# Kernel tuning notes

Measured on AMD Instinct MI355X. Metric: run time of the kernel, lower is better.

The kernel has to match this reference:

```python
import jax, jax.numpy as jnp
import numpy as np

S, B, D, H, FF, L, V, O = 512, 32, 512, 8, 2048, 6, 32000, 1000
DH = D // H
EPS = 1e-5


def layer_norm(x, g, b):
    mu = jnp.mean(x, axis=-1, keepdims=True)
    var = jnp.mean((x - mu) ** 2, axis=-1, keepdims=True)
    return (x - mu) * jax.lax.rsqrt(var + EPS) * g + b


def positional_encoding(seq_len, dim):
    pos = np.arange(seq_len, dtype=np.float32)[:, None]
    i = np.arange(dim)
    angle = pos / (10000.0 ** ((i // 2 * 2.0) / dim))
    pe = np.where(i % 2 == 0, np.sin(angle), np.cos(angle)).astype(np.float32)
    return jnp.asarray(pe)  # [seq_len, dim]


def setup_inputs() -> dict:
    key = jax.random.key(0)
    ks = jax.random.split(key, 16)
    sc = 0.02
    inp = {
        'x': jax.random.randint(ks[0], (S, B), 0, V, dtype=jnp.int32),
        'x_len': jnp.full((B,), S, dtype=jnp.int32),
        'emb': jax.random.normal(ks[1], (V, D), jnp.float32) * sc,
        'Wq': jax.random.normal(ks[2], (L, D, D), jnp.float32) * sc,
        'bq': jnp.zeros((L, D), jnp.float32),
        'Wk': jax.random.normal(ks[3], (L, D, D), jnp.float32) * sc,
        'bk': jnp.zeros((L, D), jnp.float32),
        'Wv': jax.random.normal(ks[4], (L, D, D), jnp.float32) * sc,
        'bv': jnp.zeros((L, D), jnp.float32),
        'Wo': jax.random.normal(ks[5], (L, D, D), jnp.float32) * sc,
        'bo': jnp.zeros((L, D), jnp.float32),
        'ln1_g': jnp.ones((L, D), jnp.float32),
        'ln1_b': jnp.zeros((L, D), jnp.float32),
        'W1': jax.random.normal(ks[6], (L, D, FF), jnp.float32) * sc,
        'b1': jnp.zeros((L, FF), jnp.float32),
        'W2': jax.random.normal(ks[7], (L, FF, D), jnp.float32) * sc,
        'b2': jnp.zeros((L, D), jnp.float32),
        'ln2_g': jnp.ones((L, D), jnp.float32),
        'ln2_b': jnp.zeros((L, D), jnp.float32),
        'W_fc': jax.random.normal(ks[8], (S * D, O), jnp.float32) * sc,
        'b_fc': jnp.zeros((O,), jnp.float32),
    }
    return inp


def reference(x, x_len, emb, Wq, bq, Wk, bk, Wv, bv, Wo, bo, ln1_g, ln1_b,
              W1, b1, W2, b2, ln2_g, ln2_b, W_fc, b_fc):
    out = emb[x]                      # [S, B, D]
    out = jnp.transpose(out, (1, 0, 2))  # [B, S, D]
    out = out + positional_encoding(S, D)[None, :, :]
    scale = DH ** -0.5
    for l in range(L):
        # NOTE: faithful to the original buggy head-split: plain row-major
        # reshape [B,S,D] -> [B*H,S,DH] without a [B,H,S,DH] transpose.
        q = jnp.reshape(out @ Wq[l] + bq[l], (B * H, S, DH))
        k = jnp.reshape(out @ Wk[l] + bk[l], (B * H, S, DH))
        v = jnp.reshape(out @ Wv[l] + bv[l], (B * H, S, DH))
        attn = jax.nn.softmax(jnp.einsum('gqd,gkd->gqk', q, k) * scale, axis=-1)
        ctx = jnp.einsum('gqk,gkd->gqd', attn, v).reshape(B, S, D)
        h = layer_norm(ctx @ Wo[l] + bo[l] + out, ln1_g[l], ln1_b[l])
        f = jax.nn.relu(h @ W1[l] + b1[l]) @ W2[l] + b2[l]
        out = layer_norm(f + h, ln2_g[l], ln2_b[l])
    out = out.reshape(B, S * D)
    return out @ W_fc + b_fc          # [B, O]
```

## Files before the change

### kernel.cpp

```cpp
#include <hip/hip_runtime.h>
#include <cstdint>
#include <cstddef>

#define S_  512
#define B_  32
#define D_  512
#define FF_ 2048
#define L_  6
#define O_  1000
#define M_  (B_*S_)
#define G_  256
#define DH_ 64

typedef __attribute__((ext_vector_type(8))) short bf16x8;
typedef __attribute__((ext_vector_type(4))) float f32x4;
typedef __attribute__((ext_vector_type(16))) float f32x16;

__device__ __forceinline__ unsigned short f2bf(float f) {
  unsigned int u = __builtin_bit_cast(unsigned int, f);
  u = (u + 0x7fffu + ((u >> 16) & 1u)) >> 16;
  return (unsigned short)u;
}
__device__ __forceinline__ float bf2f(unsigned short u) {
  return __builtin_bit_cast(float, (unsigned int)u << 16);
}
__device__ __forceinline__ unsigned int pkbf(float a, float b) {
  return (unsigned int)f2bf(a) | ((unsigned int)f2bf(b) << 16);
}
__device__ __forceinline__ unsigned int prm(float a, float b) {
  return __builtin_amdgcn_perm(__builtin_bit_cast(unsigned int, b),
                               __builtin_bit_cast(unsigned int, a), 0x07060302u);
}
__device__ __forceinline__ void gload_lds16(const void* g, void* l) {
  __builtin_amdgcn_global_load_lds(
      (const __attribute__((address_space(1))) unsigned int*)g,
      (__attribute__((address_space(3))) unsigned int*)l, 16, 0, 0);
}

__global__ void pe_kernel(float* __restrict__ pe) {
  int i = blockIdx.x * 256 + threadIdx.x;
  int s = i >> 9, d = i & 511;
  double de = (double)(d & ~1);
  double ang = (double)s * exp(de * (-9.210340371976184 / 512.0));
  pe[i] = (d & 1) ? (float)cos(ang) : (float)sin(ang);
}

__global__ void wconv_kernel(const float* __restrict__ W, unsigned short* __restrict__ Wt,
                             int K, int N, size_t ozs) {
  __shared__ float tile[32][33];
  const float* Wl = W + (size_t)blockIdx.z * K * N;
  unsigned short* Wtl = Wt + (size_t)blockIdx.z * ozs;
  int k0 = blockIdx.x * 32, n0 = blockIdx.y * 32;
  int c = threadIdx.x & 31, rb = threadIdx.x >> 5;
#pragma unroll
  for (int i = 0; i < 4; ++i) {
    int r = rb + i * 8;
    tile[r][c] = Wl[(size_t)(k0 + r) * N + n0 + c];
  }
  __syncthreads();
#pragma unroll
  for (int i = 0; i < 4; ++i) {
    int r = rb + i * 8;
    Wtl[(size_t)(n0 + r) * K + k0 + c] = f2bf(tile[c][r]);
  }
}

__global__ void embed_kernel(const int* __restrict__ x, const float* __restrict__ emb,
                             const float* __restrict__ pe, unsigned short* __restrict__ xb) {
  int bi = blockIdx.x;
  int s = bi / B_, b = bi % B_;
  int tok = x[s * B_ + b];
  int d = threadIdx.x * 4;
  float4 e = *(const float4*)(emb + (size_t)tok * D_ + d);
  float4 p = *(const float4*)(pe + (size_t)s * D_ + d);
  size_t o = ((size_t)b * S_ + s) * D_ + d;
  ushort4 u;
  u.x = f2bf(e.x + p.x); u.y = f2bf(e.y + p.y);
  u.z = f2bf(e.z + p.z); u.w = f2bf(e.w + p.w);
  *(ushort4*)(xb + o) = u;
}

__global__ __launch_bounds__(256, 2) void gemm_kernel(
    const unsigned short* __restrict__ A, const unsigned short* __restrict__ Bt,
    const float* __restrict__ b0, const float* __restrict__ b1, const float* __restrict__ b2,
    unsigned short* __restrict__ o0, unsigned short* __restrict__ o1, unsigned short* __restrict__ o2,
    int K, int N, int relu, int split, int nbx) {
  __shared__ unsigned short As[3][128 * 32];
  __shared__ unsigned short Bs[3][256 * 32];
  int nwg = nbx * (M_ / 128);
  int cpx = nwg >> 3;
  int id = blockIdx.x;
  int wg = (id & 7) * cpx + (id >> 3);
  int bx = wg % nbx, by = wg / nbx;
  int m0 = by * 128, n0 = bx * 256;

  int tid = threadIdx.x, lane = tid & 63, wid = tid >> 6;
  f32x4 acc[8][4];
#pragma unroll
  for (int mi = 0; mi < 8; ++mi)
#pragma unroll
    for (int ni = 0; ni < 4; ++ni) acc[mi][ni] = (f32x4)0.0f;

  int srow = lane >> 2, scol = (lane & 3) * 8;
  const unsigned short* Abase = A + (size_t)m0 * K;
  const unsigned short* Bbase = Bt + (size_t)n0 * K;
  int c16 = lane & 15, hi = lane >> 4;
  int koff = hi * 8;
  int brow = wid * 64 + c16;
  int nk = K >> 5;

  auto STAGE = [&](int kt, int bb) {
    int k0 = kt * 32;
#pragma unroll
    for (int i = 0; i < 6; ++i) {
      int c = wid * 6 + i;
      if (c < 8) {
        gload_lds16(Abase + (size_t)(c * 16 + srow) * K + k0 + scol, (char*)As[bb] + c * 1024);
      } else {
        int c2 = c - 8;
        gload_lds16(Bbase + (size_t)(c2 * 16 + srow) * K + k0 + scol, (char*)Bs[bb] + c2 * 1024);
      }
    }
  };

  STAGE(0, 0); STAGE(1, 1); STAGE(2, 2);
  int bb = 0;
  for (int kt = 0; kt < nk; ++kt) {
    int rem = nk - 1 - kt;
    if (rem >= 2)      asm volatile("s_waitcnt vmcnt(12)" ::: "memory");
    else if (rem == 1) asm volatile("s_waitcnt vmcnt(6)" ::: "memory");
    else               asm volatile("s_waitcnt vmcnt(0)" ::: "memory");
    __builtin_amdgcn_s_barrier();
    __builtin_amdgcn_sched_barrier(0);
    bf16x8 af[8], bfr[4];
#pragma unroll
    for (int mi = 0; mi < 8; ++mi) af[mi] = *(const bf16x8*)&As[bb][(mi * 16 + c16) * 32 + koff];
#pragma unroll
    for (int ni = 0; ni < 4; ++ni) bfr[ni] = *(const bf16x8*)&Bs[bb][(brow + ni * 16) * 32 + koff];
    __builtin_amdgcn_s_setprio(1);
#pragma unroll
    for (int mi = 0; mi < 8; ++mi)
#pragma unroll
      for (int ni = 0; ni < 4; ++ni)
        acc[mi][ni] = __builtin_amdgcn_mfma_f32_16x16x32_bf16(bfr[ni], af[mi], acc[mi][ni], 0, 0, 0);
    __builtin_amdgcn_s_setprio(0);
    __builtin_amdgcn_sched_barrier(0);
    __builtin_amdgcn_s_barrier();
    if (kt + 3 < nk) STAGE(kt + 3, bb);
    bb = (bb == 2) ? 0 : bb + 1;
  }

  const float* bias = b0;
  unsigned short* outb = o0;
  int nbase = n0, ostride = N;
  if (split) {
    int seg = n0 >> 9;
    if (seg == 1) { bias = b1; outb = o1; }
    else if (seg == 2) { bias = b2; outb = o2; }
    nbase = n0 & 511; ostride = 512;
  }
#pragma unroll
  for (int ni = 0; ni < 4; ++ni) {
    int colb = nbase + wid * 64 + ni * 16 + hi * 4;
    float4 bv = *(const float4*)(bias + colb);
#pragma unroll
    for (int mi = 0; mi < 8; ++mi) {
      int row = m0 + mi * 16 + c16;
      float v0 = acc[mi][ni][0] + bv.x;
      float v1 = acc[mi][ni][1] + bv.y;
      float v2 = acc[mi][ni][2] + bv.z;
      float v3 = acc[mi][ni][3] + bv.w;
      if (relu) { v0 = fmaxf(v0, 0.f); v1 = fmaxf(v1, 0.f); v2 = fmaxf(v2, 0.f); v3 = fmaxf(v3, 0.f); }
      *(uint2*)(outb + (size_t)row * ostride + colb) = make_uint2(pkbf(v0, v1), pkbf(v2, v3));
    }
  }
}

__global__ __launch_bounds__(256, 2) void gemm128_kernel(
    const unsigned short* __restrict__ A, const unsigned short* __restrict__ Bt,
    const float* __restrict__ bias, unsigned short* __restrict__ outb,
    int K, int N, int nbx) {
  __shared__ unsigned short As[3][128 * 32];
  __shared__ unsigned short Bs[3][128 * 32];
  int nwg = nbx * (M_ / 128);
  int cpx = nwg >> 3;
  int id = blockIdx.x;
  int wg = (id & 7) * cpx + (id >> 3);
  int bx = wg % nbx, by = wg / nbx;
  int m0 = by * 128, n0 = bx * 128;

  int tid = threadIdx.x, lane = tid & 63, wid = tid >> 6;
  int wm = wid >> 1, wn = wid & 1;
  f32x4 acc[4][4];
#pragma unroll
  for (int mi = 0; mi < 4; ++mi)
#pragma unroll
    for (int ni = 0; ni < 4; ++ni) acc[mi][ni] = (f32x4)0.0f;

  int srow = lane >> 2, scol = (lane & 3) * 8;
  const unsigned short* Abase = A + (size_t)m0 * K;
  const unsigned short* Bbase = Bt + (size_t)n0 * K;
  int c16 = lane & 15, hi = lane >> 4;
  int koff = hi * 8;
  int arow = wm * 64 + c16, brow = wn * 64 + c16;
  int nk = K >> 5;

  auto STAGE = [&](int kt, int bb) {
    int k0 = kt * 32;
#pragma unroll
    for (int i = 0; i < 2; ++i) {
      int c = wid * 2 + i;
      gload_lds16(Abase + (size_t)(c * 16 + srow) * K + k0 + scol, (char*)As[bb] + c * 1024);
      gload_lds16(Bbase + (size_t)(c * 16 + srow) * K + k0 + scol, (char*)Bs[bb] + c * 1024);
    }
  };

  STAGE(0, 0); STAGE(1, 1); STAGE(2, 2);
  int bb = 0;
  for (int kt = 0; kt < nk; ++kt) {
    int rem = nk - 1 - kt;
    if (rem >= 2)      asm volatile("s_waitcnt vmcnt(8)" ::: "memory");
    else if (rem == 1) asm volatile("s_waitcnt vmcnt(4)" ::: "memory");
    else               asm volatile("s_waitcnt vmcnt(0)" ::: "memory");
    __builtin_amdgcn_s_barrier();
    __builtin_amdgcn_sched_barrier(0);
    bf16x8 af[4], bfr[4];
#pragma unroll
    for (int mi = 0; mi < 4; ++mi) af[mi] = *(const bf16x8*)&As[bb][(arow + mi * 16) * 32 + koff];
#pragma unroll
    for (int ni = 0; ni < 4; ++ni) bfr[ni] = *(const bf16x8*)&Bs[bb][(brow + ni * 16) * 32 + koff];
    __builtin_amdgcn_s_setprio(1);
#pragma unroll
    for (int mi = 0; mi < 4; ++mi)
#pragma unroll
      for (int ni = 0; ni < 4; ++ni)
        acc[mi][ni] = __builtin_amdgcn_mfma_f32_16x16x32_bf16(bfr[ni], af[mi], acc[mi][ni], 0, 0, 0);
    __builtin_amdgcn_s_setprio(0);
    __builtin_amdgcn_sched_barrier(0);
    __builtin_amdgcn_s_barrier();
    if (kt + 3 < nk) STAGE(kt + 3, bb);
    bb = (bb == 2) ? 0 : bb + 1;
  }

#pragma unroll
  for (int ni = 0; ni < 4; ++ni) {
    int colb = n0 + wn * 64 + ni * 16 + hi * 4;
    float4 bv = *(const float4*)(bias + colb);
#pragma unroll
    for (int mi = 0; mi < 4; ++mi) {
      int row = m0 + wm * 64 + mi * 16 + c16;
      float v0 = acc[mi][ni][0] + bv.x;
      float v1 = acc[mi][ni][1] + bv.y;
      float v2 = acc[mi][ni][2] + bv.z;
      float v3 = acc[mi][ni][3] + bv.w;
      *(uint2*)(outb + (size_t)row * N + colb) = make_uint2(pkbf(v0, v1), pkbf(v2, v3));
    }
  }
}

__global__ __launch_bounds__(128) void addln_kernel(
    const unsigned short* __restrict__ Y, const unsigned short* __restrict__ R,
    const float* __restrict__ g, const float* __restrict__ b,
    unsigned short* __restrict__ Out) {
  __shared__ float red[2], red2[2];
  int row = blockIdx.x, t = threadIdx.x;
  size_t o = (size_t)row * 512 + t * 4;
  ushort4 yv = *(const ushort4*)(Y + o);
  ushort4 rv = *(const ushort4*)(R + o);
  float v0 = bf2f(yv.x) + bf2f(rv.x);
  float v1 = bf2f(yv.y) + bf2f(rv.y);
  float v2 = bf2f(yv.z) + bf2f(rv.z);
  float v3 = bf2f(yv.w) + bf2f(rv.w);
  float s = v0 + v1 + v2 + v3;
#pragma unroll
  for (int m = 1; m < 64; m <<= 1) s += __shfl_xor(s, m);
  if ((t & 63) == 0) red[t >> 6] = s;
  __syncthreads();
  float mean = (red[0] + red[1]) * (1.0f / 512.0f);
  float d0 = v0 - mean, d1 = v1 - mean, d2 = v2 - mean, d3 = v3 - mean;
  float sq = d0 * d0 + d1 * d1 + d2 * d2 + d3 * d3;
#pragma unroll
  for (int m = 1; m < 64; m <<= 1) sq += __shfl_xor(sq, m);
  if ((t & 63) == 0) red2[t >> 6] = sq;
  __syncthreads();
  float var = (red2[0] + red2[1]) * (1.0f / 512.0f);
  float rstd = rsqrtf(var + 1e-5f);
  float4 gg = *(const float4*)(g + t * 4);
  float4 bb = *(const float4*)(b + t * 4);
  float y0 = d0 * rstd * gg.x + bb.x;
  float y1 = d1 * rstd * gg.y + bb.y;
  float y2 = d2 * rstd * gg.z + bb.z;
  float y3 = d3 * rstd * gg.w + bb.w;
  *(uint2*)(Out + o) = make_uint2(pkbf(y0, y1), pkbf(y2, y3));
}

__global__ __launch_bounds__(256) void attn_kernel(
    const unsigned short* __restrict__ Q, const unsigned short* __restrict__ Kb,
    const unsigned short* __restrict__ Vb, unsigned short* __restrict__ Ctx) {
  __shared__ char KlB[8192];
  __shared__ char VtB[8192];
  int g = blockIdx.y;
  int q0 = blockIdx.x * 256;
  const unsigned short* Kg = Kb + (size_t)g * 512 * 64;
  const unsigned short* Vg = Vb + (size_t)g * 512 * 64;
  int tid = threadIdx.x, lane = tid & 63, wid = tid >> 6;
  int l31 = lane & 31, h = lane >> 5;
  bool lo = (lane < 32);
  int qrowA = q0 + wid * 64 + l31;
  int qrowB = qrowA + 32;
  const float sc2 = 0.125f * 1.44269504f;

  bf16x8 qfa[4], qfb[4];
  {
    const unsigned short* qpa = Q + ((size_t)g * 512 + qrowA) * 64;
    const unsigned short* qpb = Q + ((size_t)g * 512 + qrowB) * 64;
#pragma unroll
    for (int c = 0; c < 4; ++c) {
      bf16x8 ra = *(const bf16x8*)(qpa + c * 16 + h * 8);
      bf16x8 rb = *(const bf16x8*)(qpb + c * 16 + h * 8);
      union { unsigned int u[4]; bf16x8 v; } ua, ub;
#pragma unroll
      for (int j = 0; j < 4; ++j) {
        ua.u[j] = pkbf(bf2f((unsigned short)ra[2 * j]) * sc2,
                       bf2f((unsigned short)ra[2 * j + 1]) * sc2);
        ub.u[j] = pkbf(bf2f((unsigned short)rb[2 * j]) * sc2,
                       bf2f((unsigned short)rb[2 * j + 1]) * sc2);
      }
      qfa[c] = ua.v; qfb[c] = ub.v;
    }
  }

  f32x16 cA0 = (f32x16)0.0f, cA1 = (f32x16)0.0f;
  f32x16 cB0 = (f32x16)0.0f, cB1 = (f32x16)0.0f;
  float mrA = -3.0e38f, lsA = 0.0f;
  float mrB = -3.0e38f, lsB = 0.0f;

  for (int kt = 0; kt < 8; ++kt) {
    __syncthreads();
    {
      int row = tid >> 2;
      size_t base = (size_t)(kt * 64 + row) * 64;
#pragma unroll
      for (int i = 0; i < 2; ++i) {
        int cb = ((tid & 3) + 4 * i) * 16;
        bf16x8 kv = *(const bf16x8*)(Kg + base + cb / 2);
        *(bf16x8*)(KlB + row * 128 + (cb ^ ((row & 7) << 4))) = kv;
        bf16x8 vv = *(const bf16x8*)(Vg + base + cb / 2);
#pragma unroll
        for (int j = 0; j < 8; ++j) {
          int d = cb / 2 + j;
          *(unsigned short*)(VtB + d * 128 + ((2 * row) ^ ((d & 7) << 4))) =
              (unsigned short)vv[j];
        }
      }
    }
    __syncthreads();

#pragma unroll
    for (int sub = 0; sub < 2; ++sub) {
      f32x16 s0 = (f32x16)0.0f, s1 = (f32x16)0.0f;
#pragma unroll
      for (int c = 0; c < 4; ++c) {
        int cb = 32 * c + 16 * h;
        int sw = cb ^ ((l31 & 7) << 4);
        bf16x8 k0 = *(const bf16x8*)(KlB + l31 * 128 + sw);
        bf16x8 k1 = *(const bf16x8*)(KlB + (32 + l31) * 128 + sw);
        bf16x8 qf = sub ? qfb[c] : qfa[c];
        s0 = __builtin_amdgcn_mfma_f32_32x32x16_bf16(k0, qf, s0, 0, 0, 0);
        s1 = __builtin_amdgcn_mfma_f32_32x32x16_bf16(k1, qf, s1, 0, 0, 0);
      }

      float mr = sub ? mrB : mrA;
      float ls = sub ? lsB : lsA;
      float pm = s0[0];
#pragma unroll
      for (int i = 1; i < 16; ++i) pm = fmaxf(pm, s0[i]);
#pragma unroll
      for (int i = 0; i < 16; ++i) pm = fmaxf(pm, s1[i]);
      pm = fmaxf(pm, __shfl_xor(pm, 32));
      if (!__all(pm <= mr + 8.0f)) {
        float mnew = fmaxf(mr, pm);
        float alpha = exp2f(mr - mnew);
        ls *= alpha;
        if (sub) {
#pragma unroll
          for (int i = 0; i < 16; ++i) { cB0[i] *= alpha; cB1[i] *= alpha; }
        } else {
#pragma unroll
          for (int i = 0; i < 16; ++i) { cA0[i] *= alpha; cA1[i] *= alpha; }
        }
        mr = mnew;
      }
      float p[32];
      float rs = 0.0f;
#pragma unroll
      for (int i = 0; i < 16; ++i) { p[i] = exp2f(s0[i] - mr); rs += p[i]; }
#pragma unroll
      for (int i = 0; i < 16; ++i) { p[16 + i] = exp2f(s1[i] - mr); rs += p[16 + i]; }
      float rso = __shfl_xor(rs, 32);
      ls += rs + rso;
      if (sub) { mrB = mr; lsB = ls; } else { mrA = mr; lsA = ls; }

      union { unsigned int u[4]; bf16x8 v; } pa[4];
#pragma unroll
      for (int t = 0; t < 2; ++t) {
#pragma unroll
        for (int u = 0; u < 2; ++u) {
#pragma unroll
          for (int pr = 0; pr < 2; ++pr) {
            const int b0i = t * 16 + 8 * u;
            unsigned int a  = prm(p[b0i + 2 * pr],     p[b0i + 2 * pr + 1]);
            unsigned int b  = prm(p[b0i + 4 + 2 * pr], p[b0i + 4 + 2 * pr + 1]);
            unsigned int sa = __shfl_xor(a, 32);
            unsigned int sb = __shfl_xor(b, 32);
            pa[t * 2 + u].u[pr]     = lo ? a  : sb;
            pa[t * 2 + u].u[2 + pr] = lo ? sa : b;
          }
        }
      }

#pragma unroll
      for (int kc = 0; kc < 4; ++kc) {
        int cb = 32 * kc + 16 * h;
        int sw = cb ^ ((l31 & 7) << 4);
        bf16x8 v0 = *(const bf16x8*)(VtB + l31 * 128 + sw);
        bf16x8 v1 = *(const bf16x8*)(VtB + (32 + l31) * 128 + sw);
        if (sub) {
          cB0 = __builtin_amdgcn_mfma_f32_32x32x16_bf16(v0, pa[kc].v, cB0, 0, 0, 0);
          cB1 = __builtin_amdgcn_mfma_f32_32x32x16_bf16(v1, pa[kc].v, cB1, 0, 0, 0);
        } else {
          cA0 = __builtin_amdgcn_mfma_f32_32x32x16_bf16(v0, pa[kc].v, cA0, 0, 0, 0);
          cA1 = __builtin_amdgcn_mfma_f32_32x32x16_bf16(v1, pa[kc].v, cA1, 0, 0, 0);
        }
      }
    }
  }

#pragma unroll
  for (int sub = 0; sub < 2; ++sub) {
    float inv = 1.0f / (sub ? lsB : lsA);
    int qrow = sub ? qrowB : qrowA;
    unsigned short* cp = Ctx + ((size_t)g * 512 + qrow) * 64;
#pragma unroll
    for (int dh = 0; dh < 2; ++dh) {
#pragma unroll
      for (int rq = 0; rq < 4; ++rq) {
        float e0 = (sub ? (dh ? cB1[rq * 4 + 0] : cB0[rq * 4 + 0]) : (dh ? cA1[rq * 4 + 0] : cA0[rq * 4 + 0])) * inv;
        float e1 = (sub ? (dh ? cB1[rq * 4 + 1] : cB0[rq * 4 + 1]) : (dh ? cA1[rq * 4 + 1] : cA0[rq * 4 + 1])) * inv;
        float e2 = (sub ? (dh ? cB1[rq * 4 + 2] : cB0[rq * 4 + 2]) : (dh ? cA1[rq * 4 + 2] : cA0[rq * 4 + 2])) * inv;
        float e3 = (sub ? (dh ? cB1[rq * 4 + 3] : cB0[rq * 4 + 3]) : (dh ? cA1[rq * 4 + 3] : cA0[rq * 4 + 3])) * inv;
        int d0 = dh * 32 + rq * 8 + h * 4;
        *(uint2*)(cp + d0) = make_uint2(pkbf(e0, e1), pkbf(e2, e3));
      }
    }
  }
}

#define KCH 1024
__global__ __launch_bounds__(512) void fc_part_kernel(const unsigned short* __restrict__ act,
                                                      const float* __restrict__ Wfc,
                                                      float* __restrict__ part) {
  __shared__ float al[32][256];
  int t = threadIdx.x;
  int kc = blockIdx.x;
  size_t k0 = (size_t)kc * KCH;
  int o1 = t;
  int o2 = 512 + t;
  bool a2 = (o2 < O_);
  float acc1[32], acc2[32];
#pragma unroll
  for (int bb = 0; bb < 32; ++bb) { acc1[bb] = 0.0f; acc2[bb] = 0.0f; }
  for (int sub = 0; sub < KCH / 256; ++sub) {
    __syncthreads();
    for (int i = t; i < 32 * 128; i += 512) {
      int bb = i >> 7, kk = (i & 127) * 2;
      ushort2 u = *(const ushort2*)(act + (size_t)bb * 262144 + k0 + sub * 256 + kk);
      al[bb][kk] = bf2f(u.x);
      al[bb][kk + 1] = bf2f(u.y);
    }
    __syncthreads();
    const float* wp = Wfc + (k0 + sub * 256) * O_;
    for (int kk = 0; kk < 256; kk += 4) {
      const float* wr = wp + (size_t)kk * O_;
      float w10 = wr[o1];
      float w11 = wr[O_ + o1];
      float w12 = wr[2 * O_ + o1];
      float w13 = wr[3 * O_ + o1];
      float w20 = a2 ? wr[o2] : 0.0f;
      float w21 = a2 ? wr[O_ + o2] : 0.0f;
      float w22 = a2 ? wr[2 * O_ + o2] : 0.0f;
      float w23 = a2 ? wr[3 * O_ + o2] : 0.0f;
#pragma unroll
      for (int bb = 0; bb < 32; ++bb) {
        f32x4 av = *(const f32x4*)&al[bb][kk];
        acc1[bb] = fmaf(av[0], w10, acc1[bb]);
        acc1[bb] = fmaf(av[1], w11, acc1[bb]);
        acc1[bb] = fmaf(av[2], w12, acc1[bb]);
        acc1[bb] = fmaf(av[3], w13, acc1[bb]);
        acc2[bb] = fmaf(av[0], w20, acc2[bb]);
        acc2[bb] = fmaf(av[1], w21, acc2[bb]);
        acc2[bb] = fmaf(av[2], w22, acc2[bb]);
        acc2[bb] = fmaf(av[3], w23, acc2[bb]);
      }
    }
  }
#pragma unroll
  for (int bb = 0; bb < 32; ++bb) {
    part[((size_t)kc * 32 + bb) * O_ + o1] = acc1[bb];
    if (a2) part[((size_t)kc * 32 + bb) * O_ + o2] = acc2[bb];
  }
}

__global__ void fc_reduce_kernel(const float* __restrict__ part, const float* __restrict__ bfc,
                                 float* __restrict__ out) {
  int o = blockIdx.x * 256 + threadIdx.x;
  int b = blockIdx.y;
  if (o >= O_) return;
  float s = bfc[o];
  for (int c = 0; c < 256; ++c) s += part[((size_t)c * 32 + b) * O_ + o];
  out[(size_t)b * O_ + o] = s;
}

extern "C" void kernel_launch(void* const* d_in, const int* in_sizes, int n_in,
                              void* d_out, int out_size, void* d_ws, size_t ws_size,
                              hipStream_t stream) {
  const int*   x   = (const int*)d_in[0];
  const float* emb = (const float*)d_in[2];
  const float* Wq  = (const float*)d_in[3];
  const float* bq  = (const float*)d_in[4];
  const float* Wk  = (const float*)d_in[5];
  const float* bk  = (const float*)d_in[6];
  const float* Wv  = (const float*)d_in[7];
  const float* bv  = (const float*)d_in[8];
  const float* Wo  = (const float*)d_in[9];
  const float* bo  = (const float*)d_in[10];
  const float* g1  = (const float*)d_in[11];
  const float* bn1 = (const float*)d_in[12];
  const float* W1  = (const float*)d_in[13];
  const float* bf1 = (const float*)d_in[14];
  const float* W2  = (const float*)d_in[15];
  const float* bf2 = (const float*)d_in[16];
  const float* g2  = (const float*)d_in[17];
  const float* bn2 = (const float*)d_in[18];
  const float* Wfc = (const float*)d_in[19];
  const float* bfc = (const float*)d_in[20];
  float* out = (float*)d_out;

  char* ws = (char*)d_ws;
  size_t off = 0;
  auto take = [&](size_t bytes) { char* p = ws + off; off += (bytes + 255) & ~(size_t)255; return p; };
  float*          pe   = (float*)take((size_t)512 * 512 * 4);
  unsigned short* wqkv = (unsigned short*)take((size_t)L_ * 1536 * 512 * 2);
  unsigned short* wot  = (unsigned short*)take((size_t)L_ * 512 * 512 * 2);
  unsigned short* w1t  = (unsigned short*)take((size_t)L_ * 2048 * 512 * 2);
  unsigned short* w2t  = (unsigned short*)take((size_t)L_ * 512 * 2048 * 2);
  unsigned short* xb   = (unsigned short*)take((size_t)M_ * 512 * 2);
  unsigned short* qb   = (unsigned short*)take((size_t)M_ * 512 * 2);
  unsigned short* kb   = (unsigned short*)take((size_t)M_ * 512 * 2);
  unsigned short* vb   = (unsigned short*)take((size_t)M_ * 512 * 2);
  unsigned short* cxb  = (unsigned short*)take((size_t)M_ * 512 * 2);
  unsigned short* hb   = (unsigned short*)take((size_t)M_ * 512 * 2);
  unsigned short* t1   = (unsigned short*)take((size_t)M_ * 512 * 2);
  unsigned short* f1b  = qb;
  float*          part = (float*)qb;

  pe_kernel<<<1024, 256, 0, stream>>>(pe);
  wconv_kernel<<<dim3(16, 16, L_), 256, 0, stream>>>(Wq, wqkv,          512, 512,  (size_t)1536 * 512);
  wconv_kernel<<<dim3(16, 16, L_), 256, 0, stream>>>(Wk, wqkv + 262144, 512, 512,  (size_t)1536 * 512);
  wconv_kernel<<<dim3(16, 16, L_), 256, 0, stream>>>(Wv, wqkv + 524288, 512, 512,  (size_t)1536 * 512);
  wconv_kernel<<<dim3(16, 16, L_), 256, 0, stream>>>(Wo, wot,           512, 512,  (size_t)512 * 512);
  wconv_kernel<<<dim3(16, 64, L_), 256, 0, stream>>>(W1, w1t,           512, 2048, (size_t)2048 * 512);
  wconv_kernel<<<dim3(64, 16, L_), 256, 0, stream>>>(W2, w2t,           2048, 512, (size_t)512 * 2048);
  embed_kernel<<<M_, 128, 0, stream>>>(x, emb, pe, xb);

  for (int l = 0; l < L_; ++l) {
    gemm_kernel<<<768, 256, 0, stream>>>(
        xb, wqkv + (size_t)l * 1536 * 512,
        bq + l * 512, bk + l * 512, bv + l * 512,
        qb, kb, vb, 512, 1536, 0, 1, 6);
    attn_kernel<<<dim3(2, G_), 256, 0, stream>>>(qb, kb, vb, cxb);
    gemm128_kernel<<<512, 256, 0, stream>>>(
        cxb, wot + (size_t)l * 512 * 512, bo + l * 512, t1, 512, 512, 4);
    addln_kernel<<<M_, 128, 0, stream>>>(t1, xb, g1 + l * 512, bn1 + l * 512, hb);
    gemm_kernel<<<1024, 256, 0, stream>>>(
        hb, w1t + (size_t)l * 2048 * 512,
        bf1 + l * 2048, nullptr, nullptr,
        f1b, nullptr, nullptr, 512, 2048, 1, 0, 8);
    gemm128_kernel<<<512, 256, 0, stream>>>(
        f1b, w2t + (size_t)l * 512 * 2048, bf2 + l * 512, t1, 2048, 512, 4);
    addln_kernel<<<M_, 128, 0, stream>>>(t1, hb, g2 + l * 512, bn2 + l * 512, xb);
  }

  fc_part_kernel<<<256, 512, 0, stream>>>(xb, Wfc, part);
  fc_reduce_kernel<<<dim3(4, 32), 256, 0, stream>>>(part, bfc, out);
}
```

Baseline: 1.915 ms.

## Use 128x128 double-buffered GEMM for QKV and prefetch K/V tiles in attention

Moves the split QKV projection from the 128x256 triple-buffered GEMM to the 128x128 kernel, which now uses double buffering and a three-blocks-per-CU launch bound, so more workgroups fit on the device. The attention kernel now loads the next K/V tile into registers while computing on the current one, which hides global-load latency behind the MFMA work. The trade-offs are a shallower prefetch pipeline in the GEMM, tighter register limits, and more registers held in attention.

```diff
diff --git a/kernel.cpp b/kernel.cpp
--- a/kernel.cpp
+++ b/kernel.cpp
@@ -82,9 +82,8 @@
 
 __global__ __launch_bounds__(256, 2) void gemm_kernel(
     const unsigned short* __restrict__ A, const unsigned short* __restrict__ Bt,
-    const float* __restrict__ b0, const float* __restrict__ b1, const float* __restrict__ b2,
-    unsigned short* __restrict__ o0, unsigned short* __restrict__ o1, unsigned short* __restrict__ o2,
-    int K, int N, int relu, int split, int nbx) {
+    const float* __restrict__ bias, unsigned short* __restrict__ outb,
+    int K, int N, int relu, int nbx) {
   __shared__ unsigned short As[3][128 * 32];
   __shared__ unsigned short Bs[3][256 * 32];
   int nwg = nbx * (M_ / 128);
@@ -150,6 +149,88 @@
     bb = (bb == 2) ? 0 : bb + 1;
   }
 
+#pragma unroll
+  for (int ni = 0; ni < 4; ++ni) {
+    int colb = n0 + wid * 64 + ni * 16 + hi * 4;
+    float4 bv = *(const float4*)(bias + colb);
+#pragma unroll
+    for (int mi = 0; mi < 8; ++mi) {
+      int row = m0 + mi * 16 + c16;
+      float v0 = acc[mi][ni][0] + bv.x;
+      float v1 = acc[mi][ni][1] + bv.y;
+      float v2 = acc[mi][ni][2] + bv.z;
+      float v3 = acc[mi][ni][3] + bv.w;
+      if (relu) { v0 = fmaxf(v0, 0.f); v1 = fmaxf(v1, 0.f); v2 = fmaxf(v2, 0.f); v3 = fmaxf(v3, 0.f); }
+      *(uint2*)(outb + (size_t)row * N + colb) = make_uint2(pkbf(v0, v1), pkbf(v2, v3));
+    }
+  }
+}
+
+__global__ __launch_bounds__(256, 3) void gemm128_kernel(
+    const unsigned short* __restrict__ A, const unsigned short* __restrict__ Bt,
+    const float* __restrict__ b0, const float* __restrict__ b1, const float* __restrict__ b2,
+    unsigned short* __restrict__ o0, unsigned short* __restrict__ o1, unsigned short* __restrict__ o2,
+    int K, int N, int relu, int split, int nbx) {
+  __shared__ unsigned short As[2][128 * 32];
+  __shared__ unsigned short Bs[2][128 * 32];
+  int nwg = nbx * (M_ / 128);
+  int cpx = nwg >> 3;
+  int id = blockIdx.x;
+  int wg = (id & 7) * cpx + (id >> 3);
+  int bx = wg % nbx, by = wg / nbx;
+  int m0 = by * 128, n0 = bx * 128;
+
+  int tid = threadIdx.x, lane = tid & 63, wid = tid >> 6;
+  int wm = wid >> 1, wn = wid & 1;
+  f32x4 acc[4][4];
+#pragma unroll
+  for (int mi = 0; mi < 4; ++mi)
+#pragma unroll
+    for (int ni = 0; ni < 4; ++ni) acc[mi][ni] = (f32x4)0.0f;
+
+  int srow = lane >> 2, scol = (lane & 3) * 8;
+  const unsigned short* Abase = A + (size_t)m0 * K;
+  const unsigned short* Bbase = Bt + (size_t)n0 * K;
+  int c16 = lane & 15, hi = lane >> 4;
+  int koff = hi * 8;
+  int arow = wm * 64 + c16, brow = wn * 64 + c16;
+  int nk = K >> 5;
+
+  auto STAGE = [&](int kt, int bb) {
+    int k0 = kt * 32;
+#pragma unroll
+    for (int i = 0; i < 2; ++i) {
+      int c = wid * 2 + i;
+      gload_lds16(Abase + (size_t)(c * 16 + srow) * K + k0 + scol, (char*)As[bb] + c * 1024);
+      gload_lds16(Bbase + (size_t)(c * 16 + srow) * K + k0 + scol, (char*)Bs[bb] + c * 1024);
+    }
+  };
+
+  STAGE(0, 0); STAGE(1, 1);
+  int bb = 0;
+  for (int kt = 0; kt < nk; ++kt) {
+    if (kt + 1 < nk) asm volatile("s_waitcnt vmcnt(4)" ::: "memory");
+    else             asm volatile("s_waitcnt vmcnt(0)" ::: "memory");
+    __builtin_amdgcn_s_barrier();
+    __builtin_amdgcn_sched_barrier(0);
+    bf16x8 af[4], bfr[4];
+#pragma unroll
+    for (int mi = 0; mi < 4; ++mi) af[mi] = *(const bf16x8*)&As[bb][(arow + mi * 16) * 32 + koff];
+#pragma unroll
+    for (int ni = 0; ni < 4; ++ni) bfr[ni] = *(const bf16x8*)&Bs[bb][(brow + ni * 16) * 32 + koff];
+    __builtin_amdgcn_s_setprio(1);
+#pragma unroll
+    for (int mi = 0; mi < 4; ++mi)
+#pragma unroll
+      for (int ni = 0; ni < 4; ++ni)
+        acc[mi][ni] = __builtin_amdgcn_mfma_f32_16x16x32_bf16(bfr[ni], af[mi], acc[mi][ni], 0, 0, 0);
+    __builtin_amdgcn_s_setprio(0);
+    __builtin_amdgcn_sched_barrier(0);
+    __builtin_amdgcn_s_barrier();
+    if (kt + 2 < nk) STAGE(kt + 2, bb);
+    bb ^= 1;
+  }
+
   const float* bias = b0;
   unsigned short* outb = o0;
   int nbase = n0, ostride = N;
@@ -161,99 +242,17 @@
   }
 #pragma unroll
   for (int ni = 0; ni < 4; ++ni) {
-    int colb = nbase + wid * 64 + ni * 16 + hi * 4;
+    int colb = nbase + wn * 64 + ni * 16 + hi * 4;
     float4 bv = *(const float4*)(bias + colb);
 #pragma unroll
-    for (int mi = 0; mi < 8; ++mi) {
-      int row = m0 + mi * 16 + c16;
+    for (int mi = 0; mi < 4; ++mi) {
+      int row = m0 + wm * 64 + mi * 16 + c16;
       float v0 = acc[mi][ni][0] + bv.x;
       float v1 = acc[mi][ni][1] + bv.y;
       float v2 = acc[mi][ni][2] + bv.z;
       float v3 = acc[mi][ni][3] + bv.w;
       if (relu) { v0 = fmaxf(v0, 0.f); v1 = fmaxf(v1, 0.f); v2 = fmaxf(v2, 0.f); v3 = fmaxf(v3, 0.f); }
       *(uint2*)(outb + (size_t)row * ostride + colb) = make_uint2(pkbf(v0, v1), pkbf(v2, v3));
-    }
-  }
-}
-
-__global__ __launch_bounds__(256, 2) void gemm128_kernel(
-    const unsigned short* __restrict__ A, const unsigned short* __restrict__ Bt,
-    const float* __restrict__ bias, unsigned short* __restrict__ outb,
-    int K, int N, int nbx) {
-  __shared__ unsigned short As[3][128 * 32];
-  __shared__ unsigned short Bs[3][128 * 32];
-  int nwg = nbx * (M_ / 128);
-  int cpx = nwg >> 3;
-  int id = blockIdx.x;
-  int wg = (id & 7) * cpx + (id >> 3);
-  int bx = wg % nbx, by = wg / nbx;
-  int m0 = by * 128, n0 = bx * 128;
-
-  int tid = threadIdx.x, lane = tid & 63, wid = tid >> 6;
-  int wm = wid >> 1, wn = wid & 1;
-  f32x4 acc[4][4];
-#pragma unroll
-  for (int mi = 0; mi < 4; ++mi)
-#pragma unroll
-    for (int ni = 0; ni < 4; ++ni) acc[mi][ni] = (f32x4)0.0f;
-
-  int srow = lane >> 2, scol = (lane & 3) * 8;
-  const unsigned short* Abase = A + (size_t)m0 * K;
-  const unsigned short* Bbase = Bt + (size_t)n0 * K;
-  int c16 = lane & 15, hi = lane >> 4;
-  int koff = hi * 8;
-  int arow = wm * 64 + c16, brow = wn * 64 + c16;
-  int nk = K >> 5;
-
-  auto STAGE = [&](int kt, int bb) {
-    int k0 = kt * 32;
-#pragma unroll
-    for (int i = 0; i < 2; ++i) {
-      int c = wid * 2 + i;
-      gload_lds16(Abase + (size_t)(c * 16 + srow) * K + k0 + scol, (char*)As[bb] + c * 1024);
-      gload_lds16(Bbase + (size_t)(c * 16 + srow) * K + k0 + scol, (char*)Bs[bb] + c * 1024);
-    }
-  };
-
-  STAGE(0, 0); STAGE(1, 1); STAGE(2, 2);
-  int bb = 0;
-  for (int kt = 0; kt < nk; ++kt) {
-    int rem = nk - 1 - kt;
-    if (rem >= 2)      asm volatile("s_waitcnt vmcnt(8)" ::: "memory");
-    else if (rem == 1) asm volatile("s_waitcnt vmcnt(4)" ::: "memory");
-    else               asm volatile("s_waitcnt vmcnt(0)" ::: "memory");
-    __builtin_amdgcn_s_barrier();
-    __builtin_amdgcn_sched_barrier(0);
-    bf16x8 af[4], bfr[4];
-#pragma unroll
-    for (int mi = 0; mi < 4; ++mi) af[mi] = *(const bf16x8*)&As[bb][(arow + mi * 16) * 32 + koff];
-#pragma unroll
-    for (int ni = 0; ni < 4; ++ni) bfr[ni] = *(const bf16x8*)&Bs[bb][(brow + ni * 16) * 32 + koff];
-    __builtin_amdgcn_s_setprio(1);
-#pragma unroll
-    for (int mi = 0; mi < 4; ++mi)
-#pragma unroll
-      for (int ni = 0; ni < 4; ++ni)
-        acc[mi][ni] = __builtin_amdgcn_mfma_f32_16x16x32_bf16(bfr[ni], af[mi], acc[mi][ni], 0, 0, 0);
-    __builtin_amdgcn_s_setprio(0);
-    __builtin_amdgcn_sched_barrier(0);
-    __builtin_amdgcn_s_barrier();
-    if (kt + 3 < nk) STAGE(kt + 3, bb);
-    bb = (bb == 2) ? 0 : bb + 1;
-  }
-
-#pragma unroll
-  for (int ni = 0; ni < 4; ++ni) {
-    int colb = n0 + wn * 64 + ni * 16 + hi * 4;
-    float4 bv = *(const float4*)(bias + colb);
-#pragma unroll
-    for (int mi = 0; mi < 4; ++mi) {
-      int row = m0 + wm * 64 + mi * 16 + c16;
-      float v0 = acc[mi][ni][0] + bv.x;
-      float v1 = acc[mi][ni][1] + bv.y;
-      float v2 = acc[mi][ni][2] + bv.z;
-      float v3 = acc[mi][ni][3] + bv.w;
-      *(uint2*)(outb + (size_t)row * N + colb) = make_uint2(pkbf(v0, v1), pkbf(v2, v3));
     }
   }
 }
@@ -335,24 +334,35 @@
   float mrA = -3.0e38f, lsA = 0.0f;
   float mrB = -3.0e38f, lsB = 0.0f;
 
+  int rowS = tid >> 2;
+  int cbA = (tid & 3) * 16;
+  int cbB = cbA + 64;
+  int swA = cbA ^ ((rowS & 7) << 4);
+  int swB = cbB ^ ((rowS & 7) << 4);
+
+  bf16x8 kc0 = *(const bf16x8*)(Kg + (size_t)rowS * 64 + cbA / 2);
+  bf16x8 kc1 = *(const bf16x8*)(Kg + (size_t)rowS * 64 + cbB / 2);
+  bf16x8 vc0 = *(const bf16x8*)(Vg + (size_t)rowS * 64 + cbA / 2);
+  bf16x8 vc1 = *(const bf16x8*)(Vg + (size_t)rowS * 64 + cbB / 2);
+
   for (int kt = 0; kt < 8; ++kt) {
     __syncthreads();
-    {
-      int row = tid >> 2;
-      size_t base = (size_t)(kt * 64 + row) * 64;
-#pragma unroll
-      for (int i = 0; i < 2; ++i) {
-        int cb = ((tid & 3) + 4 * i) * 16;
-        bf16x8 kv = *(const bf16x8*)(Kg + base + cb / 2);
-        *(bf16x8*)(KlB + row * 128 + (cb ^ ((row & 7) << 4))) = kv;
-        bf16x8 vv = *(const bf16x8*)(Vg + base + cb / 2);
-#pragma unroll
-        for (int j = 0; j < 8; ++j) {
-          int d = cb / 2 + j;
-          *(unsigned short*)(VtB + d * 128 + ((2 * row) ^ ((d & 7) << 4))) =
-              (unsigned short)vv[j];
-        }
-      }
+    *(bf16x8*)(KlB + rowS * 128 + swA) = kc0;
+    *(bf16x8*)(KlB + rowS * 128 + swB) = kc1;
+#pragma unroll
+    for (int j = 0; j < 8; ++j) {
+      int dA = cbA / 2 + j;
+      int dB = cbB / 2 + j;
+      *(unsigned short*)(VtB + dA * 128 + ((2 * rowS) ^ ((dA & 7) << 4))) = (unsigned short)vc0[j];
+      *(unsigned short*)(VtB + dB * 128 + ((2 * rowS) ^ ((dB & 7) << 4))) = (unsigned short)vc1[j];
+    }
+    bf16x8 kn0, kn1, vn0, vn1;
+    if (kt < 7) {
+      size_t nb = (size_t)((kt + 1) * 64 + rowS) * 64;
+      kn0 = *(const bf16x8*)(Kg + nb + cbA / 2);
+      kn1 = *(const bf16x8*)(Kg + nb + cbB / 2);
+      vn0 = *(const bf16x8*)(Vg + nb + cbA / 2);
+      vn1 = *(const bf16x8*)(Vg + nb + cbB / 2);
     }
     __syncthreads();
 
@@ -434,6 +444,8 @@
         }
       }
     }
+
+    if (kt < 7) { kc0 = kn0; kc1 = kn1; vc0 = vn0; vc1 = vn1; }
   }
 
 #pragma unroll
@@ -574,20 +586,22 @@
   embed_kernel<<<M_, 128, 0, stream>>>(x, emb, pe, xb);
 
   for (int l = 0; l < L_; ++l) {
-    gemm_kernel<<<768, 256, 0, stream>>>(
+    gemm128_kernel<<<1536, 256, 0, stream>>>(
         xb, wqkv + (size_t)l * 1536 * 512,
         bq + l * 512, bk + l * 512, bv + l * 512,
-        qb, kb, vb, 512, 1536, 0, 1, 6);
+        qb, kb, vb, 512, 1536, 0, 1, 12);
     attn_kernel<<<dim3(2, G_), 256, 0, stream>>>(qb, kb, vb, cxb);
     gemm128_kernel<<<512, 256, 0, stream>>>(
-        cxb, wot + (size_t)l * 512 * 512, bo + l * 512, t1, 512, 512, 4);
+        cxb, wot + (size_t)l * 512 * 512,
+        bo + l * 512, nullptr, nullptr,
+        t1, nullptr, nullptr, 512, 512, 0, 0, 4);
     addln_kernel<<<M_, 128, 0, stream>>>(t1, xb, g1 + l * 512, bn1 + l * 512, hb);
     gemm_kernel<<<1024, 256, 0, stream>>>(
-        hb, w1t + (size_t)l * 2048 * 512,
-        bf1 + l * 2048, nullptr, nullptr,
-        f1b, nullptr, nullptr, 512, 2048, 1, 0, 8);
+        hb, w1t + (size_t)l * 2048 * 512, bf1 + l * 2048, f1b, 512, 2048, 1, 8);
     gemm128_kernel<<<512, 256, 0, stream>>>(
-        f1b, w2t + (size_t)l * 512 * 2048, bf2 + l * 512, t1, 2048, 512, 4);
+        f1b, w2t + (size_t)l * 512 * 2048,
+        bf2 + l * 512, nullptr, nullptr,
+        t1, nullptr, nullptr, 2048, 512, 0, 0, 4);
     addln_kernel<<<M_, 128, 0, stream>>>(t1, hb, g2 + l * 512, bn2 + l * 512, xb);
   }
 
```

Result: faster. 1.872 ms (-2.3%).
